# Performance work log

Measured on AMD Instinct MI355X. Metric: run time of the kernel, lower is better.

The kernel has to match this reference:

```python
import jax, jax.numpy as jnp
import numpy as np

B, L, D, NL, VOCAB = 2, 8192, 512, 8, 32
FFT_LEN = 2 * L  # causal linear conv via zero-padded FFT


def layernorm(x, g, b, eps=1e-5):
    mu = jnp.mean(x, axis=-1, keepdims=True)
    var = jnp.var(x, axis=-1, keepdims=True)
    return (x - mu) * jax.lax.rsqrt(var + eps) * g + b


def fftconv(v, h, bias):
    # v: [B, d, L], h: [d, L] long implicit filter, bias: [d] skip (the Hyena 'D' term)
    vf = jnp.fft.rfft(v, n=FFT_LEN)
    hf = jnp.fft.rfft(h, n=FFT_LEN)
    y = jnp.fft.irfft(vf * hf[None], n=FFT_LEN)[..., :L]
    return y + v * bias[:, None]


def short_conv(p, w, b):
    # causal depthwise conv, kernel size 3: p [B, C, L], w [C, 3], b [C]
    pp = jnp.pad(p, ((0, 0), (0, 0), (2, 0)))
    out = jax.lax.conv_general_dilated(pp, w[:, None, :], (1,), 'VALID',
                                       feature_group_count=p.shape[1])
    return out + b[None, :, None]


def setup_inputs() -> dict:
    key = jax.random.key(0)
    ks = jax.random.split(key, 12)
    rn = lambda k, sh, s: jax.random.normal(k, sh, jnp.float32) * s
    d = D
    return {
        'input_ids': jax.random.randint(ks[0], (B, L), 0, VOCAB),
        'emb': rn(ks[1], (VOCAB, d), 0.02),
        'ln1_g': jnp.ones((NL, d)), 'ln1_b': jnp.zeros((NL, d)),
        'Win': rn(ks[2], (NL, d, 3 * d), d ** -0.5), 'bin_': jnp.zeros((NL, 3 * d)),
        'convw': rn(ks[3], (NL, 3 * d, 3), 3 ** -0.5), 'convb': jnp.zeros((NL, 3 * d)),
        'h': rn(ks[4], (NL, d, L), L ** -0.5),  # implicit long filter, materialized
        'Db': rn(ks[5], (NL, d), 1.0),
        'Wout': rn(ks[6], (NL, d, d), d ** -0.5), 'bout': jnp.zeros((NL, d)),
        'ln2_g': jnp.ones((NL, d)), 'ln2_b': jnp.zeros((NL, d)),
        'W1': rn(ks[7], (NL, d, 4 * d), d ** -0.5), 'b1': jnp.zeros((NL, 4 * d)),
        'W2': rn(ks[8], (NL, 4 * d, d), (4 * d) ** -0.5), 'b2': jnp.zeros((NL, d)),
        'lnf_g': jnp.ones((d,)), 'lnf_b': jnp.zeros((d,)),
    }


def reference(input_ids, emb, ln1_g, ln1_b, Win, bin_, convw, convb, h, Db,
              Wout, bout, ln2_g, ln2_b, W1, b1, W2, b2, lnf_g, lnf_b):
    u = emb[input_ids]  # [B, L, d]
    for l in range(NL):  # structural loop over layers
        z = layernorm(u, ln1_g[l], ln1_b[l])
        p = (jnp.einsum('bld,de->ble', z, Win[l]) + bin_[l]).transpose(0, 2, 1)  # [B,3d,L]
        p = short_conv(p, convw[l], convb[l])
        x2, x1, v = jnp.split(p, 3, axis=1)  # each [B, d, L]
        v = fftconv(v * x1, h[l], Db[l])     # gate then FFT long conv (order-2 Hyena)
        y = (v * x2).transpose(0, 2, 1)      # output gate -> [B, L, d]
        u = u + jnp.einsum('bld,de->ble', y, Wout[l]) + bout[l]
        z = layernorm(u, ln2_g[l], ln2_b[l])
        hmid = jax.nn.gelu(jnp.einsum('bld,df->blf', z, W1[l]) + b1[l])
        u = u + jnp.einsum('blf,fd->bld', hmid, W2[l]) + b2[l]
    return layernorm(u, lnf_g, lnf_b)  # last_hidden_state [B, L, d]
```

## Files before the change

kernel.cpp:

```cpp
#include <hip/hip_runtime.h>
#include <hip/hip_bf16.h>
#include <math.h>

#define BB 2
#define LL 8192
#define DD 512
#define NLAYER 8
#define TD 1536
#define HD 2048
#define NFFT 16384
#define NHALF 8192
#define HSTR 4160
#define BLD (BB*LL*DD)
#define BLH ((size_t)BB*LL*HD)

typedef unsigned short u16;
typedef unsigned int   u32;
typedef __bf16 bf16x8 __attribute__((ext_vector_type(8)));
typedef float  f32x4  __attribute__((ext_vector_type(4)));

__device__ __forceinline__ u16 f2bf(float f) {
    union { float f; u32 u; } v; v.f = f;
    u32 r = v.u + 0x7FFF + ((v.u >> 16) & 1);
    return (u16)(r >> 16);
}
__device__ __forceinline__ float bf2f(u16 h) {
    union { u32 u; float f; } v; v.u = (u32)h << 16; return v.f;
}

__device__ __forceinline__ void async_g2l_16(const u16* g, u16* l) {
    __builtin_amdgcn_global_load_lds(
        (const __attribute__((address_space(1))) void*)g,
        (__attribute__((address_space(3))) void*)l,
        16, 0, 0);
}

__device__ __forceinline__ float2 cmul(float2 a, float2 b) {
    return make_float2(a.x * b.x - a.y * b.y, a.x * b.y + a.y * b.x);
}
__device__ __forceinline__ float2 cmulc(float2 a, float2 b) {
    return make_float2(a.x * b.x + a.y * b.y, a.y * b.x - a.x * b.y);
}
__device__ __forceinline__ float2 cadd(float2 a, float2 b) {
    return make_float2(a.x + b.x, a.y + b.y);
}
__device__ __forceinline__ float2 csub(float2 a, float2 b) {
    return make_float2(a.x - b.x, a.y - b.y);
}
__device__ __forceinline__ int drev12(int m) {
    return ((m & 3) << 10) | (((m >> 2) & 3) << 8) | (((m >> 4) & 3) << 6) |
           (((m >> 6) & 3) << 4) | (((m >> 8) & 3) << 2) | ((m >> 10) & 3);
}
__device__ __forceinline__ int perm8k(int k) {
    return ((k & 1) << 12) + drev12(k >> 1);
}
__device__ __forceinline__ int swz(int i) {
    return i ^ (((i >> 4) ^ (i >> 8)) & 15);
}
#define LDX(arr, i) arr[swz(i)]

__global__ void twiddle_kernel(float* twf) {
    int k = blockIdx.x * 256 + threadIdx.x;
    if (k < NFFT) {
        double ang = -2.0 * M_PI * (double)k / (double)NFFT;
        twf[2 * k]     = (float)cos(ang);
        twf[2 * k + 1] = (float)sin(ang);
    }
}

__global__ void embed_kernel(const int* __restrict__ ids,
                             const float* __restrict__ emb,
                             float* __restrict__ u) {
    int i = blockIdx.x * 256 + threadIdx.x;
    if (i < BLD) {
        int row = i >> 9;
        int d   = i & (DD - 1);
        u[i] = emb[ids[row] * DD + d];
    }
}

__global__ __launch_bounds__(256)
void wprep_kernel(const float* __restrict__ W, u16* __restrict__ WtH,
                  u16* __restrict__ WtL, int K, int N, long srcStride, long dstStride) {
    __shared__ float t[64][65];
    const float* src = W + (size_t)blockIdx.z * srcStride;
    u16* dsth = WtH + (size_t)blockIdx.z * dstStride;
    u16* dstl = WtL + (size_t)blockIdx.z * dstStride;
    int n0 = blockIdx.x * 64, k0 = blockIdx.y * 64;
    int tc = threadIdx.x & 63, tr = threadIdx.x >> 6;
    for (int r = tr; r < 64; r += 4)
        t[r][tc] = src[(size_t)(k0 + r) * N + n0 + tc];
    __syncthreads();
    for (int r = tr; r < 64; r += 4) {
        float v = t[tc][r];
        u16 h = f2bf(v);
        dsth[(size_t)(n0 + r) * K + k0 + tc] = h;
        dstl[(size_t)(n0 + r) * K + k0 + tc] = f2bf(v - bf2f(h));
    }
}

template<int MODE>
__global__ __launch_bounds__(128)
void ln_kernel(const float* __restrict__ x, void* __restrict__ out,
               void* __restrict__ outL,
               const float* __restrict__ g, const float* __restrict__ b) {
    int row = blockIdx.x;
    const float4* xr = (const float4*)(x + (size_t)row * DD);
    int t = threadIdx.x;
    float4 v = xr[t];
    float s  = v.x + v.y + v.z + v.w;
    float ss = v.x * v.x + v.y * v.y + v.z * v.z + v.w * v.w;
    for (int off = 32; off; off >>= 1) {
        s  += __shfl_down(s, off);
        ss += __shfl_down(ss, off);
    }
    __shared__ float sm[4];
    if ((t & 63) == 0) { sm[(t >> 6) * 2] = s; sm[(t >> 6) * 2 + 1] = ss; }
    __syncthreads();
    float S = sm[0] + sm[2], SS = sm[1] + sm[3];
    float mu  = S * (1.0f / DD);
    float var = SS * (1.0f / DD) - mu * mu;
    float rs  = rsqrtf(var + 1e-5f);
    float4 gg = ((const float4*)g)[t];
    float4 bb = ((const float4*)b)[t];
    float o[4];
    o[0] = (v.x - mu) * rs * gg.x + bb.x;
    o[1] = (v.y - mu) * rs * gg.y + bb.y;
    o[2] = (v.z - mu) * rs * gg.z + bb.z;
    o[3] = (v.w - mu) * rs * gg.w + bb.w;
    if (MODE == 1) {
        u16 h[4], lo[4];
#pragma unroll
        for (int i = 0; i < 4; i++) {
            h[i]  = f2bf(o[i]);
            lo[i] = f2bf(o[i] - bf2f(h[i]));
        }
        uint2 ph, pl;
        ph.x = (u32)h[0] | ((u32)h[1] << 16);  ph.y = (u32)h[2] | ((u32)h[3] << 16);
        pl.x = (u32)lo[0] | ((u32)lo[1] << 16); pl.y = (u32)lo[2] | ((u32)lo[3] << 16);
        ((uint2*)((u16*)out  + (size_t)row * DD))[t] = ph;
        ((uint2*)((u16*)outL + (size_t)row * DD))[t] = pl;
    } else {
        float4 of = {o[0], o[1], o[2], o[3]};
        ((float4*)((float*)out + (size_t)row * DD))[t] = of;
    }
}

__device__ __forceinline__ float gelu_f(float x) {
    float x3 = x * x * x;
    float t  = tanhf(0.79788456080286541f * (x + 0.044715f * x3));
    return 0.5f * x * (1.0f + t);
}

template<int OUT, bool GELU, int PASSES>
__global__ __launch_bounds__(256)
void mfma_gemm3(const u16* __restrict__ Ah, const u16* __restrict__ Al,
                const u16* __restrict__ Bh, const u16* __restrict__ Bl,
                const float* __restrict__ bias,
                float* __restrict__ Cf, u16* __restrict__ Ch, u16* __restrict__ Cl,
                int M, int N, int K) {
    __shared__ u16 AsH[128 * 32];
    __shared__ u16 AsL[128 * 32];
    __shared__ u16 BsH[128 * 32];
    __shared__ u16 BsL[(PASSES == 3) ? 128 * 32 : 8];
    int m0 = blockIdx.y * 128, n0 = blockIdx.x * 128;
    int tid = threadIdx.x;
    int w = tid >> 6, l = tid & 63;
    int wr = w >> 1, wc = w & 1;

    int ch0 = w * 2, ch1 = ch0 + 1;
    size_t offA0 = (size_t)(m0 + ch0 * 16 + (l >> 2)) * K + (l & 3) * 8;
    size_t offA1 = (size_t)(m0 + ch1 * 16 + (l >> 2)) * K + (l & 3) * 8;
    size_t offB0 = (size_t)(n0 + ch0 * 16 + (l >> 2)) * K + (l & 3) * 8;
    size_t offB1 = (size_t)(n0 + ch1 * 16 + (l >> 2)) * K + (l & 3) * 8;

    f32x4 acc[4][4] = {};
    int arow = wr * 64 + (l & 15);
    int brow = wc * 64 + (l & 15);
    int kc   = (l >> 4) * 8;

    for (int k0 = 0; k0 < K; k0 += 32) {
        async_g2l_16(Ah + offA0 + k0, &AsH[ch0 * 512]);
        async_g2l_16(Ah + offA1 + k0, &AsH[ch1 * 512]);
        async_g2l_16(Al + offA0 + k0, &AsL[ch0 * 512]);
        async_g2l_16(Al + offA1 + k0, &AsL[ch1 * 512]);
        async_g2l_16(Bh + offB0 + k0, &BsH[ch0 * 512]);
        async_g2l_16(Bh + offB1 + k0, &BsH[ch1 * 512]);
        if (PASSES == 3) {
            async_g2l_16(Bl + offB0 + k0, &BsL[ch0 * 512]);
            async_g2l_16(Bl + offB1 + k0, &BsL[ch1 * 512]);
        }
        __syncthreads();
        bf16x8 ah[4], al[4], bh[4], bl[4];
#pragma unroll
        for (int i = 0; i < 4; i++) {
            ah[i] = *(const bf16x8*)&AsH[(arow + i * 16) * 32 + kc];
            al[i] = *(const bf16x8*)&AsL[(arow + i * 16) * 32 + kc];
            bh[i] = *(const bf16x8*)&BsH[(brow + i * 16) * 32 + kc];
            if (PASSES == 3)
                bl[i] = *(const bf16x8*)&BsL[(brow + i * 16) * 32 + kc];
        }
#pragma unroll
        for (int mi = 0; mi < 4; mi++)
#pragma unroll
            for (int ni = 0; ni < 4; ni++) {
                acc[mi][ni] = __builtin_amdgcn_mfma_f32_16x16x32_bf16(
                    ah[mi], bh[ni], acc[mi][ni], 0, 0, 0);
                acc[mi][ni] = __builtin_amdgcn_mfma_f32_16x16x32_bf16(
                    al[mi], bh[ni], acc[mi][ni], 0, 0, 0);
                if (PASSES == 3)
                    acc[mi][ni] = __builtin_amdgcn_mfma_f32_16x16x32_bf16(
                        ah[mi], bl[ni], acc[mi][ni], 0, 0, 0);
            }
        __syncthreads();
    }

    int lr = l >> 4, lc = l & 15;
#pragma unroll
    for (int mi = 0; mi < 4; mi++) {
#pragma unroll
        for (int ni = 0; ni < 4; ni++) {
            int col = n0 + wc * 64 + ni * 16 + lc;
            float bv = bias[col];
            int rowb = m0 + wr * 64 + mi * 16 + lr * 4;
#pragma unroll
            for (int r = 0; r < 4; r++) {
                float v = acc[mi][ni][r] + bv;
                if (GELU) v = gelu_f(v);
                size_t off = (size_t)(rowb + r) * N + col;
                if (OUT == 0) {
                    Cf[off] = v;
                } else if (OUT == 1) {
                    u16 h = f2bf(v);
                    Ch[off] = h;
                    Cl[off] = f2bf(v - bf2f(h));
                } else {
                    Cf[off] += v;
                }
            }
        }
    }
}

__global__ __launch_bounds__(256)
void conv_gate_kernel(const float* __restrict__ p, const float* __restrict__ cw,
                      const float* __restrict__ cb, float* __restrict__ vg,
                      float* __restrict__ x2s) {
    __shared__ float tvg[64][65];
    __shared__ float tx2[64][65];
    int b = blockIdx.z, c0 = blockIdx.y * 64, l0 = blockIdx.x * 64;
    int tc = threadIdx.x & 63, tr = threadIdx.x >> 6;
    const float* pb = p + (size_t)b * LL * TD;
    int cx2 = c0 + tc;
    int cx1 = DD + c0 + tc;
    int cv  = 2 * DD + c0 + tc;
    float w20 = cw[cx2 * 3], w21 = cw[cx2 * 3 + 1], w22 = cw[cx2 * 3 + 2], bx2 = cb[cx2];
    float w10 = cw[cx1 * 3], w11 = cw[cx1 * 3 + 1], w12 = cw[cx1 * 3 + 2], bx1 = cb[cx1];
    float wv0 = cw[cv * 3],  wv1 = cw[cv * 3 + 1],  wv2 = cw[cv * 3 + 2],  bv  = cb[cv];
    for (int r = tr; r < 64; r += 4) {
        int l = l0 + r;
        size_t o0 = (size_t)l * TD;
        float p2a = (l >= 2) ? pb[o0 - 2 * TD + cx2] : 0.f;
        float p1a = (l >= 1) ? pb[o0 - TD + cx2] : 0.f;
        float p0a = pb[o0 + cx2];
        float p2b = (l >= 2) ? pb[o0 - 2 * TD + cx1] : 0.f;
        float p1b = (l >= 1) ? pb[o0 - TD + cx1] : 0.f;
        float p0b = pb[o0 + cx1];
        float p2c = (l >= 2) ? pb[o0 - 2 * TD + cv] : 0.f;
        float p1c = (l >= 1) ? pb[o0 - TD + cv] : 0.f;
        float p0c = pb[o0 + cv];
        float x2v = w20 * p2a + w21 * p1a + w22 * p0a + bx2;
        float x1v = w10 * p2b + w11 * p1b + w12 * p0b + bx1;
        float vv  = wv0 * p2c + wv1 * p1c + wv2 * p0c + bv;
        tx2[r][tc] = x2v;
        tvg[r][tc] = vv * x1v;
    }
    __syncthreads();
    for (int r = tr; r < 64; r += 4) {
        size_t o = ((size_t)b * DD + c0 + r) * LL + l0 + tc;
        vg[o]  = tvg[tc][r];
        x2s[o] = tx2[tc][r];
    }
}

__global__ __launch_bounds__(256)
void ytr_kernel(const float* __restrict__ yg, u16* __restrict__ yh,
                u16* __restrict__ yl) {
    __shared__ float t[64][65];
    int b = blockIdx.z, c0 = blockIdx.y * 64, l0 = blockIdx.x * 64;
    int tc = threadIdx.x & 63, tr = threadIdx.x >> 6;
    for (int r = tr; r < 64; r += 4)
        t[r][tc] = yg[((size_t)b * DD + c0 + r) * LL + l0 + tc];
    __syncthreads();
    for (int r = tr; r < 64; r += 4) {
        float v = t[tc][r];
        u16 h = f2bf(v);
        size_t o = ((size_t)(b * LL + l0 + r)) * DD + c0 + tc;
        yh[o] = h;
        yl[o] = f2bf(v - bf2f(h));
    }
}

__device__ __forceinline__ void fft8192_fwd(float2* ld, const float2* __restrict__ tw, int tid) {
    __syncthreads();
    for (int n = tid; n < 4096; n += 1024) {
        float2 a = LDX(ld, n), b = LDX(ld, n + 4096);
        LDX(ld, n) = cadd(a, b);
        float2 d = csub(a, b);
        LDX(ld, n + 4096) = n ? cmul(d, tw[2 * n]) : d;
    }
    for (int s = 0; s < 6; s++) {
        int lm = 12 - 2 * s, lq = lm - 2;
        int Q = 1 << lq;
        __syncthreads();
        for (int g = tid; g < 2048; g += 1024) {
            int half = g >> 10, gg = g & 1023;
            int j = gg & (Q - 1);
            int base = (half << 12) + ((gg >> lq) << lm) + j;
            float2 x0 = LDX(ld, base), x1 = LDX(ld, base + Q);
            float2 x2 = LDX(ld, base + 2 * Q), x3 = LDX(ld, base + 3 * Q);
            float2 a = cadd(x0, x2), b = csub(x0, x2);
            float2 c = cadd(x1, x3), d = csub(x1, x3);
            float2 mid = make_float2(d.y, -d.x);
            float2 u0 = cadd(a, c);
            float2 u1 = cadd(b, mid);
            float2 u2 = csub(a, c);
            float2 u3 = csub(b, mid);
            int e = j << (2 * s);
            if (e) {
                u1 = cmul(u1, tw[4 * e]);
                u2 = cmul(u2, tw[8 * e]);
                u3 = cmul(u3, tw[12 * e]);
            }
            LDX(ld, base) = u0; LDX(ld, base + Q) = u1;
            LDX(ld, base + 2 * Q) = u2; LDX(ld, base + 3 * Q) = u3;
        }
    }
    __syncthreads();
}

__device__ __forceinline__ void fft8192_inv(float2* ld, const float2* __restrict__ tw, int tid) {
    for (int s = 5; s >= 0; s--) {
        int lm = 12 - 2 * s, lq = lm - 2;
        int Q = 1 << lq;
        __syncthreads();
        for (int g = tid; g < 2048; g += 1024) {
            int half = g >> 10, gg = g & 1023;
            int j = gg & (Q - 1);
            int base = (half << 12) + ((gg >> lq) << lm) + j;
            int e = j << (2 * s);
            float2 v0 = LDX(ld, base);
            float2 v1 = LDX(ld, base + Q), v2 = LDX(ld, base + 2 * Q), v3 = LDX(ld, base + 3 * Q);
            if (e) {
                v1 = cmulc(v1, tw[4 * e]);
                v2 = cmulc(v2, tw[8 * e]);
                v3 = cmulc(v3, tw[12 * e]);
            }
            float2 a = cadd(v0, v2), b = csub(v0, v2);
            float2 c = cadd(v1, v3), d = csub(v1, v3);
            float2 id = make_float2(-d.y, d.x);
            LDX(ld, base)         = cadd(a, c);
            LDX(ld, base + Q)     = cadd(b, id);
            LDX(ld, base + 2 * Q) = csub(a, c);
            LDX(ld, base + 3 * Q) = csub(b, id);
        }
    }
    __syncthreads();
    for (int n = tid; n < 4096; n += 1024) {
        float2 a = LDX(ld, n);
        float2 b = LDX(ld, n + 4096);
        if (n) b = cmulc(b, tw[2 * n]);
        LDX(ld, n) = cadd(a, b);
        LDX(ld, n + 4096) = csub(a, b);
    }
    __syncthreads();
}

__global__ __launch_bounds__(1024, 8)
void hf_kernel(const float* __restrict__ h, float2* __restrict__ HfA,
               float2* __restrict__ HfB, const float* __restrict__ twf) {
    __shared__ float2 ld[NHALF];
    int c = blockIdx.x;
    const float2* hp = (const float2*)(h + (size_t)c * LL);
    const float2* tw = (const float2*)twf;
    int tid = threadIdx.x;
    for (int n = tid; n < 4096; n += 1024) LDX(ld, n) = hp[n];
    for (int n = 4096 + tid; n < NHALF; n += 1024) LDX(ld, n) = make_float2(0.f, 0.f);
    fft8192_fwd(ld, tw, tid);
    float2* oa = HfA + (size_t)c * HSTR;
    float2* ob = HfB + (size_t)c * HSTR;
    for (int k = tid; k <= 4096; k += 1024) {
        int kc = (NHALF - k) & (NHALF - 1);
        int p = perm8k(k), pc = perm8k(kc);
        float2 A = LDX(ld, p), B = LDX(ld, pc);
        float2 E = make_float2(0.5f * (A.x + B.x), 0.5f * (A.y - B.y));
        float2 O = make_float2(0.5f * (A.y + B.y), -0.5f * (A.x - B.x));
        float2 t = tw[k];
        float2 tO = cmul(t, O);
        oa[k] = cadd(E, tO);
        ob[k] = csub(E, tO);
    }
}

__global__ __launch_bounds__(1024, 8)
void fftconv_kernel(const float* __restrict__ vg, const float* __restrict__ x2s,
                    const float2* __restrict__ HfA, const float2* __restrict__ HfB,
                    const float* __restrict__ Db, const float* __restrict__ twf,
                    float* __restrict__ yg) {
    __shared__ float2 ld[NHALF];
    int bc = blockIdx.x;
    int c  = bc & (DD - 1);
    const float2* vp  = (const float2*)(vg  + (size_t)bc * LL);
    const float2* x2p = (const float2*)(x2s + (size_t)bc * LL);
    float2*       op  = (float2*)(yg + (size_t)bc * LL);
    const float2* tw = (const float2*)twf;
    int tid = threadIdx.x;
    float2 vv[4];
#pragma unroll
    for (int q = 0; q < 4; q++) {
        int n = tid + q * 1024;
        vv[q] = vp[n];
        LDX(ld, n) = vv[q];
    }
#pragma unroll
    for (int q = 0; q < 4; q++) LDX(ld, tid + 4096 + q * 1024) = make_float2(0.f, 0.f);
    fft8192_fwd(ld, tw, tid);
    const float2* Ha = HfA + (size_t)c * HSTR;
    const float2* Hb = HfB + (size_t)c * HSTR;
    for (int k = tid; k <= 4096; k += 1024) {
        int kc = (NHALF - k) & (NHALF - 1);
        int p = perm8k(k), pc = perm8k(kc);
        float2 A = LDX(ld, p), B = LDX(ld, pc);
        float2 E = make_float2(0.5f * (A.x + B.x), 0.5f * (A.y - B.y));
        float2 O = make_float2(0.5f * (A.y + B.y), -0.5f * (A.x - B.x));
        float2 t = tw[k];
        float2 tO = cmul(t, O);
        float2 X1 = cadd(E, tO);
        float2 X2 = csub(E, tO);
        float2 Hak = Ha[k], Hbk = Hb[k];
        float2 Y1 = cmul(X1, Hak);
        float2 Y2 = cmul(X2, Hbk);
        float2 S  = make_float2(0.5f * (Y1.x + Y2.x), 0.5f * (Y1.y + Y2.y));
        float2 Dd = make_float2(0.5f * (Y1.x - Y2.x), 0.5f * (Y1.y - Y2.y));
        LDX(ld, p) = cadd(S, cmul(make_float2(t.y, t.x), Dd));
        if (kc != k) {
            float2 X1c = make_float2(X2.x, -X2.y);
            float2 X2c = make_float2(X1.x, -X1.y);
            float2 Y1c = cmulc(X1c, Hbk);
            float2 Y2c = cmulc(X2c, Hak);
            float2 Sc = make_float2(0.5f * (Y1c.x + Y2c.x), 0.5f * (Y1c.y + Y2c.y));
            float2 Dc = make_float2(0.5f * (Y1c.x - Y2c.x), 0.5f * (Y1c.y - Y2c.y));
            LDX(ld, pc) = cadd(Sc, cmul(make_float2(t.y, -t.x), Dc));
        }
    }
    fft8192_inv(ld, tw, tid);
    float db = Db[c];
    const float inv = 1.0f / (float)NHALF;
#pragma unroll
    for (int q = 0; q < 4; q++) {
        int n = tid + q * 1024;
        float2 w  = LDX(ld, n);
        float2 xx = x2p[n];
        float y0 = w.x * inv + vv[q].x * db;
        float y1 = w.y * inv + vv[q].y * db;
        op[n] = make_float2(y0 * xx.x, y1 * xx.y);
    }
}

extern "C" void kernel_launch(void* const* d_in, const int* in_sizes, int n_in,
                              void* d_out, int out_size, void* d_ws, size_t ws_size,
                              hipStream_t stream) {
    const int*   ids   = (const int*)  d_in[0];
    const float* emb   = (const float*)d_in[1];
    const float* ln1_g = (const float*)d_in[2];
    const float* ln1_b = (const float*)d_in[3];
    const float* Win   = (const float*)d_in[4];
    const float* bin_  = (const float*)d_in[5];
    const float* convw = (const float*)d_in[6];
    const float* convb = (const float*)d_in[7];
    const float* hflt  = (const float*)d_in[8];
    const float* Db    = (const float*)d_in[9];
    const float* Wout  = (const float*)d_in[10];
    const float* bout  = (const float*)d_in[11];
    const float* ln2_g = (const float*)d_in[12];
    const float* ln2_b = (const float*)d_in[13];
    const float* W1    = (const float*)d_in[14];
    const float* b1    = (const float*)d_in[15];
    const float* W2    = (const float*)d_in[16];
    const float* b2    = (const float*)d_in[17];
    const float* lnf_g = (const float*)d_in[18];
    const float* lnf_b = (const float*)d_in[19];

    char* p_ = (char*)d_ws;
    auto alloc = [&](size_t bytes) {
        char* r = p_; p_ += (bytes + 255) & ~(size_t)255; return r;
    };
    float* u   = (float*)alloc((size_t)BLD * 4);
    u16* zh    = (u16*)  alloc((size_t)BLD * 2);
    u16* zl    = (u16*)  alloc((size_t)BLD * 2);
    char* uni  = alloc(2 * BLH * 2);
    float* pf  = (float*)uni;
    float* yg  = (float*)uni;
    u16* hmh   = (u16*)uni;
    u16* hml   = hmh + BLH;
    float* vg  = (float*)alloc((size_t)BLD * 4);
    float* x2s = (float*)alloc((size_t)BLD * 4);
    u16* yh    = (u16*)  alloc((size_t)BLD * 2);
    u16* yl    = (u16*)  alloc((size_t)BLD * 2);
    float2* HfA = (float2*)alloc((size_t)DD * HSTR * 8);
    float2* HfB = (float2*)alloc((size_t)DD * HSTR * 8);
    float* tw  = (float*)alloc((size_t)2 * NFFT * 4);
    u16* WtInH = (u16*)alloc((size_t)NLAYER * TD * DD * 2);
    u16* WtInL = (u16*)alloc((size_t)NLAYER * TD * DD * 2);
    u16* WtOutH= (u16*)alloc((size_t)NLAYER * DD * DD * 2);
    u16* WtOutL= (u16*)alloc((size_t)NLAYER * DD * DD * 2);
    u16* Wt1H  = (u16*)alloc((size_t)NLAYER * DD * HD * 2);
    u16* Wt1L  = (u16*)alloc((size_t)NLAYER * DD * HD * 2);
    u16* Wt2H  = (u16*)alloc((size_t)NLAYER * HD * DD * 2);
    u16* Wt2L  = (u16*)alloc((size_t)NLAYER * HD * DD * 2);

    twiddle_kernel<<<(NFFT + 255) / 256, 256, 0, stream>>>(tw);
    embed_kernel<<<(BLD + 255) / 256, 256, 0, stream>>>(ids, emb, u);
    wprep_kernel<<<dim3(TD / 64, DD / 64, NLAYER), 256, 0, stream>>>(
        Win, WtInH, WtInL, DD, TD, (long)DD * TD, (long)TD * DD);
    wprep_kernel<<<dim3(DD / 64, DD / 64, NLAYER), 256, 0, stream>>>(
        Wout, WtOutH, WtOutL, DD, DD, (long)DD * DD, (long)DD * DD);
    wprep_kernel<<<dim3(HD / 64, DD / 64, NLAYER), 256, 0, stream>>>(
        W1, Wt1H, Wt1L, DD, HD, (long)DD * HD, (long)DD * HD);
    wprep_kernel<<<dim3(DD / 64, HD / 64, NLAYER), 256, 0, stream>>>(
        W2, Wt2H, Wt2L, HD, DD, (long)HD * DD, (long)HD * DD);

    for (int l = 0; l < NLAYER; l++) {
        ln_kernel<1><<<BB * LL, 128, 0, stream>>>(u, zh, zl,
            ln1_g + l * DD, ln1_b + l * DD);

        mfma_gemm3<0, false, 3><<<dim3(TD / 128, (BB * LL) / 128), 256, 0, stream>>>(
            zh, zl, WtInH + (size_t)l * TD * DD, WtInL + (size_t)l * TD * DD,
            bin_ + (size_t)l * TD, pf, nullptr, nullptr, BB * LL, TD, DD);

        conv_gate_kernel<<<dim3(LL / 64, DD / 64, BB), 256, 0, stream>>>(
            pf, convw + (size_t)l * TD * 3, convb + (size_t)l * TD, vg, x2s);

        hf_kernel<<<DD, 1024, 0, stream>>>(hflt + (size_t)l * DD * LL, HfA, HfB, tw);

        fftconv_kernel<<<BB * DD, 1024, 0, stream>>>(
            vg, x2s, HfA, HfB, Db + (size_t)l * DD, tw, yg);

        ytr_kernel<<<dim3(LL / 64, DD / 64, BB), 256, 0, stream>>>(yg, yh, yl);

        mfma_gemm3<2, false, 2><<<dim3(DD / 128, (BB * LL) / 128), 256, 0, stream>>>(
            yh, yl, WtOutH + (size_t)l * DD * DD, WtOutL + (size_t)l * DD * DD,
            bout + (size_t)l * DD, u, nullptr, nullptr, BB * LL, DD, DD);

        ln_kernel<1><<<BB * LL, 128, 0, stream>>>(u, zh, zl,
            ln2_g + l * DD, ln2_b + l * DD);

        mfma_gemm3<1, true, 2><<<dim3(HD / 128, (BB * LL) / 128), 256, 0, stream>>>(
            zh, zl, Wt1H + (size_t)l * DD * HD, Wt1L + (size_t)l * DD * HD,
            b1 + (size_t)l * HD, nullptr, hmh, hml, BB * LL, HD, DD);

        mfma_gemm3<2, false, 2><<<dim3(DD / 128, (BB * LL) / 128), 256, 0, stream>>>(
            hmh, hml, Wt2H + (size_t)l * HD * DD, Wt2L + (size_t)l * HD * DD,
            b2 + (size_t)l * DD, u, nullptr, nullptr, BB * LL, DD, HD);
    }

    ln_kernel<0><<<BB * LL, 128, 0, stream>>>(u, (float*)d_out, nullptr, lnf_g, lnf_b);
}
```

Measured before the change: 4.988 ms.

## Replace radix-2/4 FFT passes with register radix-8 stages and shuffle final stage

Restructures the 8192-point complex FFT from a radix-2 pass plus six radix-4 LDS passes into four radix-8 register passes plus a final radix-2 done with lane shuffles, with a matching inverse. The first forward pass now loads straight from global memory into registers, and the last inverse pass feeds the epilogue from registers. Both changes cut LDS round trips and __syncthreads barriers. The output permutation changes from a base-4 digit reversal to a base-8 one, which must match the new stage order exactly. Each thread now holds 8 complex values, which raises register pressure in 1024-thread blocks.

```diff
diff --git a/kernel.cpp b/kernel.cpp
--- a/kernel.cpp
+++ b/kernel.cpp
@@ -47,12 +47,12 @@
 __device__ __forceinline__ float2 csub(float2 a, float2 b) {
     return make_float2(a.x - b.x, a.y - b.y);
 }
-__device__ __forceinline__ int drev12(int m) {
-    return ((m & 3) << 10) | (((m >> 2) & 3) << 8) | (((m >> 4) & 3) << 6) |
-           (((m >> 6) & 3) << 4) | (((m >> 8) & 3) << 2) | ((m >> 10) & 3);
-}
-__device__ __forceinline__ int perm8k(int k) {
-    return ((k & 1) << 12) + drev12(k >> 1);
+__device__ __forceinline__ int r3(int x) {
+    return ((x & 1) << 2) | (x & 2) | ((x >> 2) & 1);
+}
+__device__ __forceinline__ int perm8(int k) {
+    return (r3(k & 7) << 10) | (r3((k >> 3) & 7) << 7) | (r3((k >> 6) & 7) << 4) |
+           (r3((k >> 9) & 7) << 1) | ((k >> 12) & 1);
 }
 __device__ __forceinline__ int swz(int i) {
     return i ^ (((i >> 4) ^ (i >> 8)) & 15);
@@ -301,77 +301,137 @@
     }
 }
 
-__device__ __forceinline__ void fft8192_fwd(float2* ld, const float2* __restrict__ tw, int tid) {
-    __syncthreads();
-    for (int n = tid; n < 4096; n += 1024) {
-        float2 a = LDX(ld, n), b = LDX(ld, n + 4096);
-        LDX(ld, n) = cadd(a, b);
+__device__ __forceinline__ void r8_fwd(float2* y, const float2* __restrict__ tw,
+                                       int j, int Q, int F) {
+#pragma unroll
+    for (int t = 0; t < 4; t++) {
+        float2 a = y[t], b = y[t + 4];
+        y[t] = cadd(a, b);
         float2 d = csub(a, b);
-        LDX(ld, n + 4096) = n ? cmul(d, tw[2 * n]) : d;
-    }
-    for (int s = 0; s < 6; s++) {
-        int lm = 12 - 2 * s, lq = lm - 2;
-        int Q = 1 << lq;
-        __syncthreads();
-        for (int g = tid; g < 2048; g += 1024) {
-            int half = g >> 10, gg = g & 1023;
-            int j = gg & (Q - 1);
-            int base = (half << 12) + ((gg >> lq) << lm) + j;
-            float2 x0 = LDX(ld, base), x1 = LDX(ld, base + Q);
-            float2 x2 = LDX(ld, base + 2 * Q), x3 = LDX(ld, base + 3 * Q);
-            float2 a = cadd(x0, x2), b = csub(x0, x2);
-            float2 c = cadd(x1, x3), d = csub(x1, x3);
-            float2 mid = make_float2(d.y, -d.x);
-            float2 u0 = cadd(a, c);
-            float2 u1 = cadd(b, mid);
-            float2 u2 = csub(a, c);
-            float2 u3 = csub(b, mid);
-            int e = j << (2 * s);
-            if (e) {
-                u1 = cmul(u1, tw[4 * e]);
-                u2 = cmul(u2, tw[8 * e]);
-                u3 = cmul(u3, tw[12 * e]);
-            }
-            LDX(ld, base) = u0; LDX(ld, base + Q) = u1;
-            LDX(ld, base + 2 * Q) = u2; LDX(ld, base + 3 * Q) = u3;
-        }
-    }
-    __syncthreads();
-}
-
-__device__ __forceinline__ void fft8192_inv(float2* ld, const float2* __restrict__ tw, int tid) {
-    for (int s = 5; s >= 0; s--) {
-        int lm = 12 - 2 * s, lq = lm - 2;
-        int Q = 1 << lq;
-        __syncthreads();
-        for (int g = tid; g < 2048; g += 1024) {
-            int half = g >> 10, gg = g & 1023;
-            int j = gg & (Q - 1);
-            int base = (half << 12) + ((gg >> lq) << lm) + j;
-            int e = j << (2 * s);
-            float2 v0 = LDX(ld, base);
-            float2 v1 = LDX(ld, base + Q), v2 = LDX(ld, base + 2 * Q), v3 = LDX(ld, base + 3 * Q);
-            if (e) {
-                v1 = cmulc(v1, tw[4 * e]);
-                v2 = cmulc(v2, tw[8 * e]);
-                v3 = cmulc(v3, tw[12 * e]);
-            }
-            float2 a = cadd(v0, v2), b = csub(v0, v2);
-            float2 c = cadd(v1, v3), d = csub(v1, v3);
-            float2 id = make_float2(-d.y, d.x);
-            LDX(ld, base)         = cadd(a, c);
-            LDX(ld, base + Q)     = cadd(b, id);
-            LDX(ld, base + 2 * Q) = csub(a, c);
-            LDX(ld, base + 3 * Q) = csub(b, id);
-        }
-    }
-    __syncthreads();
-    for (int n = tid; n < 4096; n += 1024) {
-        float2 a = LDX(ld, n);
-        float2 b = LDX(ld, n + 4096);
-        if (n) b = cmulc(b, tw[2 * n]);
-        LDX(ld, n) = cadd(a, b);
-        LDX(ld, n + 4096) = csub(a, b);
+        int e = F * (j + t * Q);
+        y[t + 4] = e ? cmul(d, tw[e]) : d;
+    }
+#pragma unroll
+    for (int h = 0; h < 8; h += 4)
+#pragma unroll
+        for (int t = 0; t < 2; t++) {
+            float2 a = y[h + t], b = y[h + t + 2];
+            y[h + t] = cadd(a, b);
+            float2 d = csub(a, b);
+            int e = 2 * F * (j + t * Q);
+            y[h + t + 2] = e ? cmul(d, tw[e]) : d;
+        }
+    int ec = 4 * F * j;
+#pragma unroll
+    for (int q = 0; q < 8; q += 2) {
+        float2 a = y[q], b = y[q + 1];
+        y[q] = cadd(a, b);
+        float2 d = csub(a, b);
+        y[q + 1] = ec ? cmul(d, tw[ec]) : d;
+    }
+}
+
+__device__ __forceinline__ void r8_inv(float2* y, const float2* __restrict__ tw,
+                                       int j, int Q, int F) {
+    int ec = 4 * F * j;
+#pragma unroll
+    for (int q = 0; q < 8; q += 2) {
+        float2 b = ec ? cmulc(y[q + 1], tw[ec]) : y[q + 1];
+        float2 a = y[q];
+        y[q] = cadd(a, b); y[q + 1] = csub(a, b);
+    }
+#pragma unroll
+    for (int h = 0; h < 8; h += 4)
+#pragma unroll
+        for (int t = 0; t < 2; t++) {
+            int e = 2 * F * (j + t * Q);
+            float2 b = e ? cmulc(y[h + t + 2], tw[e]) : y[h + t + 2];
+            float2 a = y[h + t];
+            y[h + t] = cadd(a, b); y[h + t + 2] = csub(a, b);
+        }
+#pragma unroll
+    for (int t = 0; t < 4; t++) {
+        int e = F * (j + t * Q);
+        float2 b = e ? cmulc(y[t + 4], tw[e]) : y[t + 4];
+        float2 a = y[t];
+        y[t] = cadd(a, b); y[t + 4] = csub(a, b);
+    }
+}
+
+__device__ __forceinline__ void r2_shfl(float2* y, int j) {
+#pragma unroll
+    for (int t = 0; t < 8; t++) {
+        float2 o;
+        o.x = __shfl_xor(y[t].x, 1);
+        o.y = __shfl_xor(y[t].y, 1);
+        y[t] = (j == 0) ? cadd(y[t], o) : csub(o, y[t]);
+    }
+}
+
+__device__ __forceinline__ void fft_fwd_mid(float2* ld, const float2* __restrict__ tw, int tid) {
+    {
+        int j = tid & 127, base = ((tid >> 7) << 10) + j;
+        float2 y[8];
+#pragma unroll
+        for (int t = 0; t < 8; t++) y[t] = LDX(ld, base + t * 128);
+        r8_fwd(y, tw, j, 128, 16);
+#pragma unroll
+        for (int t = 0; t < 8; t++) LDX(ld, base + t * 128) = y[t];
+    }
+    __syncthreads();
+    {
+        int j = tid & 15, base = ((tid >> 4) << 7) + j;
+        float2 y[8];
+#pragma unroll
+        for (int t = 0; t < 8; t++) y[t] = LDX(ld, base + t * 16);
+        r8_fwd(y, tw, j, 16, 128);
+#pragma unroll
+        for (int t = 0; t < 8; t++) LDX(ld, base + t * 16) = y[t];
+    }
+    __syncthreads();
+    {
+        int j = tid & 1, base = ((tid >> 1) << 4) + j;
+        float2 y[8];
+#pragma unroll
+        for (int t = 0; t < 8; t++) y[t] = LDX(ld, base + t * 2);
+        r8_fwd(y, tw, j, 2, 1024);
+        r2_shfl(y, j);
+#pragma unroll
+        for (int t = 0; t < 8; t++) LDX(ld, base + t * 2) = y[t];
+    }
+    __syncthreads();
+}
+
+__device__ __forceinline__ void fft_inv_mid(float2* ld, const float2* __restrict__ tw, int tid) {
+    {
+        int j = tid & 1, base = ((tid >> 1) << 4) + j;
+        float2 y[8];
+#pragma unroll
+        for (int t = 0; t < 8; t++) y[t] = LDX(ld, base + t * 2);
+        r2_shfl(y, j);
+        r8_inv(y, tw, j, 2, 1024);
+#pragma unroll
+        for (int t = 0; t < 8; t++) LDX(ld, base + t * 2) = y[t];
+    }
+    __syncthreads();
+    {
+        int j = tid & 15, base = ((tid >> 4) << 7) + j;
+        float2 y[8];
+#pragma unroll
+        for (int t = 0; t < 8; t++) y[t] = LDX(ld, base + t * 16);
+        r8_inv(y, tw, j, 16, 128);
+#pragma unroll
+        for (int t = 0; t < 8; t++) LDX(ld, base + t * 16) = y[t];
+    }
+    __syncthreads();
+    {
+        int j = tid & 127, base = ((tid >> 7) << 10) + j;
+        float2 y[8];
+#pragma unroll
+        for (int t = 0; t < 8; t++) y[t] = LDX(ld, base + t * 128);
+        r8_inv(y, tw, j, 128, 16);
+#pragma unroll
+        for (int t = 0; t < 8; t++) LDX(ld, base + t * 128) = y[t];
     }
     __syncthreads();
 }
@@ -384,14 +444,23 @@
     const float2* hp = (const float2*)(h + (size_t)c * LL);
     const float2* tw = (const float2*)twf;
     int tid = threadIdx.x;
-    for (int n = tid; n < 4096; n += 1024) LDX(ld, n) = hp[n];
-    for (int n = 4096 + tid; n < NHALF; n += 1024) LDX(ld, n) = make_float2(0.f, 0.f);
-    fft8192_fwd(ld, tw, tid);
+    {
+        float2 y[8];
+#pragma unroll
+        for (int t = 0; t < 4; t++) y[t] = hp[tid + t * 1024];
+#pragma unroll
+        for (int t = 4; t < 8; t++) y[t] = make_float2(0.f, 0.f);
+        r8_fwd(y, tw, tid, 1024, 2);
+#pragma unroll
+        for (int t = 0; t < 8; t++) LDX(ld, tid + t * 1024) = y[t];
+    }
+    __syncthreads();
+    fft_fwd_mid(ld, tw, tid);
     float2* oa = HfA + (size_t)c * HSTR;
     float2* ob = HfB + (size_t)c * HSTR;
     for (int k = tid; k <= 4096; k += 1024) {
         int kc = (NHALF - k) & (NHALF - 1);
-        int p = perm8k(k), pc = perm8k(kc);
+        int p = perm8(k), pc = perm8(kc);
         float2 A = LDX(ld, p), B = LDX(ld, pc);
         float2 E = make_float2(0.5f * (A.x + B.x), 0.5f * (A.y - B.y));
         float2 O = make_float2(0.5f * (A.y + B.y), -0.5f * (A.x - B.x));
@@ -416,20 +485,23 @@
     const float2* tw = (const float2*)twf;
     int tid = threadIdx.x;
     float2 vv[4];
-#pragma unroll
-    for (int q = 0; q < 4; q++) {
-        int n = tid + q * 1024;
-        vv[q] = vp[n];
-        LDX(ld, n) = vv[q];
-    }
-#pragma unroll
-    for (int q = 0; q < 4; q++) LDX(ld, tid + 4096 + q * 1024) = make_float2(0.f, 0.f);
-    fft8192_fwd(ld, tw, tid);
+    {
+        float2 y[8];
+#pragma unroll
+        for (int t = 0; t < 4; t++) { vv[t] = vp[tid + t * 1024]; y[t] = vv[t]; }
+#pragma unroll
+        for (int t = 4; t < 8; t++) y[t] = make_float2(0.f, 0.f);
+        r8_fwd(y, tw, tid, 1024, 2);
+#pragma unroll
+        for (int t = 0; t < 8; t++) LDX(ld, tid + t * 1024) = y[t];
+    }
+    __syncthreads();
+    fft_fwd_mid(ld, tw, tid);
     const float2* Ha = HfA + (size_t)c * HSTR;
     const float2* Hb = HfB + (size_t)c * HSTR;
     for (int k = tid; k <= 4096; k += 1024) {
         int kc = (NHALF - k) & (NHALF - 1);
-        int p = perm8k(k), pc = perm8k(kc);
+        int p = perm8(k), pc = perm8(kc);
         float2 A = LDX(ld, p), B = LDX(ld, pc);
         float2 E = make_float2(0.5f * (A.x + B.x), 0.5f * (A.y - B.y));
         float2 O = make_float2(0.5f * (A.y + B.y), -0.5f * (A.x - B.x));
@@ -453,17 +525,23 @@
             LDX(ld, pc) = cadd(Sc, cmul(make_float2(t.y, -t.x), Dc));
         }
     }
-    fft8192_inv(ld, tw, tid);
-    float db = Db[c];
-    const float inv = 1.0f / (float)NHALF;
-#pragma unroll
-    for (int q = 0; q < 4; q++) {
-        int n = tid + q * 1024;
-        float2 w  = LDX(ld, n);
-        float2 xx = x2p[n];
-        float y0 = w.x * inv + vv[q].x * db;
-        float y1 = w.y * inv + vv[q].y * db;
-        op[n] = make_float2(y0 * xx.x, y1 * xx.y);
+    __syncthreads();
+    fft_inv_mid(ld, tw, tid);
+    {
+        float2 y[8];
+#pragma unroll
+        for (int t = 0; t < 8; t++) y[t] = LDX(ld, tid + t * 1024);
+        r8_inv(y, tw, tid, 1024, 2);
+        float db = Db[c];
+        const float inv = 1.0f / (float)NHALF;
+#pragma unroll
+        for (int t = 0; t < 4; t++) {
+            int n = tid + t * 1024;
+            float2 xx = x2p[n];
+            float y0 = y[t].x * inv + vv[t].x * db;
+            float y1 = y[t].y * inv + vv[t].y * db;
+            op[n] = make_float2(y0 * xx.x, y1 * xx.y);
+        }
     }
 }
 
```

Result: slower. 5.889 ms (+18.1%).
